# Kernel optimization log

Hardware: AMD Instinct MI355X
Metric: run time of the kernel (lower is better)

Reference implementation:

```python
import jax, jax.numpy as jnp
import numpy as np

N, E = 50000, 800000
IN_DIM, OUT_DIM, REL_DIM = 128, 64, 32
NEG_SLOPE = 0.01  # torch F.leaky_relu default


def setup_inputs() -> dict:
    key = jax.random.key(0)
    ks = jax.random.split(key, 12)
    return {
        "h": jax.random.normal(ks[0], (N, IN_DIM), jnp.float32),
        "relation": jax.random.normal(ks[1], (E, REL_DIM), jnp.float32),
        "score": jax.random.normal(ks[2], (E, 1), jnp.float32),
        "timestamp": jax.random.normal(ks[3], (E, 1), jnp.float32),
        "src": jax.random.randint(ks[4], (E,), 0, N, jnp.int32),
        "dst": jax.random.randint(ks[5], (E,), 0, N, jnp.int32),
        "W_n": jax.random.normal(ks[6], (IN_DIM, OUT_DIM), jnp.float32) / np.sqrt(IN_DIM),
        "W_r": jax.random.normal(ks[7], (REL_DIM, OUT_DIM), jnp.float32) / np.sqrt(REL_DIM),
        "W_s": jax.random.normal(ks[8], (1, OUT_DIM), jnp.float32),
        "W_t": jax.random.normal(ks[9], (1, OUT_DIM), jnp.float32),
        "a": jax.random.normal(ks[10], (5 * OUT_DIM,), jnp.float32) / np.sqrt(5 * OUT_DIM),
    }


def reference(h, relation, score, timestamp, src, dst, W_n, W_r, W_s, W_t, a):
    D = W_n.shape[1]
    z = h @ W_n                     # (N, D)
    er = relation @ W_r             # (E, D)
    es = score @ W_s                # (E, D)
    et = timestamp @ W_t            # (E, D)
    z_src = z[src]                  # (E, D) gather
    z_dst = z[dst]                  # (E, D) gather
    # attn_fc on concat([z_src, z_dst, er, es, et]) == sum of slice dot-products
    a1, a2, a3, a4, a5 = (a[0:D], a[D:2*D], a[2*D:3*D], a[3*D:4*D], a[4*D:5*D])
    logit = z_src @ a1 + z_dst @ a2 + er @ a3 + es @ a4 + et @ a5  # (E,)
    logit = jnp.where(logit >= 0, logit, NEG_SLOPE * logit)        # leaky_relu
    # segment softmax over edges grouped by dst node
    n = z.shape[0]
    seg_max = jax.ops.segment_max(logit, dst, num_segments=n)     # (N,)
    ex = jnp.exp(logit - seg_max[dst])                             # (E,)
    seg_sum = jax.ops.segment_sum(ex, dst, num_segments=n)        # (N,)
    alpha = ex / seg_sum[dst]                                      # (E,)
    # weighted scatter-sum of source features to dst nodes
    h_out = jax.ops.segment_sum(alpha[:, None] * z_src, dst, num_segments=n)  # (N, D)
    return h_out
```

## Files before the change

kernel.cpp:

```cpp
#include <hip/hip_runtime.h>

#define IN_DIM 128
#define OUT_DIM 64
#define REL_DIM 32
#define NEG_SLOPE 0.01f
#define CAP 64

__global__ void k_consts(const float* __restrict__ W_r, const float* __restrict__ W_s,
                         const float* __restrict__ W_t, const float* __restrict__ a,
                         float* __restrict__ consts ) {
    int t = threadIdx.x;
    if (t < REL_DIM) {
        const float* a3 = a + 2 * OUT_DIM;
        float acc = 0.f;
        for (int d = 0; d < OUT_DIM; ++d) acc += W_r[t * OUT_DIM + d] * a3[d];
        consts[t] = acc;
    } else if (t == 32) {
        float acc = 0.f;
        for (int d = 0; d < OUT_DIM; ++d) acc += W_s[d] * a[3 * OUT_DIM + d];
        consts[32] = acc;
    } else if (t == 33) {
        float acc = 0.f;
        for (int d = 0; d < OUT_DIM; ++d) acc += W_t[d] * a[4 * OUT_DIM + d];
        consts[33] = acc;
    }
}

__global__ __launch_bounds__(256) void k_node(const float* __restrict__ h,
                                              const float* __restrict__ W_n,
                                              const float* __restrict__ a,
                                              float* __restrict__ z,
                                              float* __restrict__ s1,
                                              float* __restrict__ s2, int n) {
    __shared__ float hs[IN_DIM * 65];
    __shared__ float s1p[4][64], s2p[4][64];
    int base = blockIdx.x * 64;

    for (int i = threadIdx.x; i < 64 * 32; i += 256) {
        int r = i >> 5;
        int c4 = i & 31;
        float4 v = make_float4(0.f, 0.f, 0.f, 0.f);
        if (base + r < n) v = ((const float4*)(h + (size_t)(base + r) * IN_DIM))[c4];
        int k0 = c4 * 4;
        hs[(k0 + 0) * 65 + r] = v.x;
        hs[(k0 + 1) * 65 + r] = v.y;
        hs[(k0 + 2) * 65 + r] = v.z;
        hs[(k0 + 3) * 65 + r] = v.w;
    }
    __syncthreads();

    int lane = threadIdx.x & 63;
    int w = __builtin_amdgcn_readfirstlane(threadIdx.x >> 6);
    int c0 = w * 16;
    int row = base + lane;

    float acc[16];
    #pragma unroll
    for (int j = 0; j < 16; ++j) acc[j] = 0.f;

    const float* __restrict__ Wslice = W_n + c0;
    #pragma unroll 4
    for (int k = 0; k < IN_DIM; ++k) {
        float hv = hs[k * 65 + lane];
        const float* __restrict__ Wr = Wslice + k * OUT_DIM;
        #pragma unroll
        for (int j = 0; j < 16; ++j) acc[j] = fmaf(hv, Wr[j], acc[j]);
    }

    float p1 = 0.f, p2 = 0.f;
    #pragma unroll
    for (int j = 0; j < 16; ++j) {
        p1 = fmaf(acc[j], a[c0 + j], p1);
        p2 = fmaf(acc[j], a[OUT_DIM + c0 + j], p2);
    }
    s1p[w][lane] = p1;
    s2p[w][lane] = p2;

    if (row < n) {
        float4* zp = (float4*)(z + (size_t)row * OUT_DIM + c0);
        zp[0] = make_float4(acc[0], acc[1], acc[2], acc[3]);
        zp[1] = make_float4(acc[4], acc[5], acc[6], acc[7]);
        zp[2] = make_float4(acc[8], acc[9], acc[10], acc[11]);
        zp[3] = make_float4(acc[12], acc[13], acc[14], acc[15]);
    }
    __syncthreads();
    if (threadIdx.x < 64 && base + (int)threadIdx.x < n) {
        int l = threadIdx.x;
        s1[base + l] = s1p[0][l] + s1p[1][l] + s1p[2][l] + s1p[3][l];
        s2[base + l] = s2p[0][l] + s2p[1][l] + s2p[2][l] + s2p[3][l];
    }
}

__global__ __launch_bounds__(256) void k_fill(const float* __restrict__ rel,
                                              const float* __restrict__ score,
                                              const float* __restrict__ ts,
                                              const int* __restrict__ src,
                                              const int* __restrict__ dst,
                                              const float* __restrict__ s1,
                                              const float* __restrict__ s2,
                                              const float* __restrict__ consts,
                                              int* __restrict__ cnt,
                                              int2* __restrict__ pedge, int E) {
    int tid = blockIdx.x * 256 + threadIdx.x;
    int e = tid >> 3;
    int sub = tid & 7;
    if (e >= E) return;

    float4 w = ((const float4*)consts)[sub];
    float4 v = ((const float4*)rel)[(size_t)e * 8 + sub];
    float dot = v.x * w.x + v.y * w.y + v.z * w.z + v.w * w.w;
    dot += __shfl_xor(dot, 1, 8);
    dot += __shfl_xor(dot, 2, 8);
    dot += __shfl_xor(dot, 4, 8);

    if (sub == 0) {
        int s = src[e], d = dst[e];
        float lg = dot + s1[s] + s2[d] + score[e] * consts[32] + ts[e] * consts[33];
        lg = (lg >= 0.f) ? lg : NEG_SLOPE * lg;
        int rank = atomicAdd(cnt + d, 1);
        if (rank < CAP)
            pedge[((size_t)d << 6) + rank] = make_int2(s, __float_as_int(lg));
    }
}

__global__ __launch_bounds__(256) void k_out(const int* __restrict__ cnt,
                                             const int2* __restrict__ pedge,
                                             const float* __restrict__ z,
                                             float* __restrict__ out, int n) {
    int lane = threadIdx.x & 63;
    int wave = (blockIdx.x * blockDim.x + threadIdx.x) >> 6;
    int nwaves = (gridDim.x * blockDim.x) >> 6;
    int eg = lane >> 4;
    int dl = lane & 15;
    for (int node = wave; node < n; node += nwaves) {
        int deg = min(cnt[node], CAP);
        float4 acc = make_float4(0.f, 0.f, 0.f, 0.f);
        if (deg > 0) {
            int2 pe = make_int2(0, (int)0xff800000u);
            if (lane < deg) pe = pedge[((size_t)node << 6) + lane];
            float v = __int_as_float(pe.y);
            float m = v;
            #pragma unroll
            for (int o = 32; o > 0; o >>= 1) m = fmaxf(m, __shfl_xor(m, o, 64));
            float ex = __expf(v - m);
            float ssum = ex;
            #pragma unroll
            for (int o = 32; o > 0; o >>= 1) ssum += __shfl_xor(ssum, o, 64);
            float alpha = ex * (1.0f / ssum);
            for (int j0 = 0; j0 < deg; j0 += 4) {
                int j = j0 + eg;
                int jc = (j < 64) ? j : 63;
                float wj = __shfl(alpha, jc, 64);
                int  sj = __shfl(pe.x, jc, 64);
                if (j < deg) {
                    float4 zv = ((const float4*)(z + (size_t)sj * OUT_DIM))[dl];
                    acc.x = fmaf(wj, zv.x, acc.x);
                    acc.y = fmaf(wj, zv.y, acc.y);
                    acc.z = fmaf(wj, zv.z, acc.z);
                    acc.w = fmaf(wj, zv.w, acc.w);
                }
            }
        }
        #pragma unroll
        for (int o = 16; o <= 32; o <<= 1) {
            acc.x += __shfl_xor(acc.x, o, 64);
            acc.y += __shfl_xor(acc.y, o, 64);
            acc.z += __shfl_xor(acc.z, o, 64);
            acc.w += __shfl_xor(acc.w, o, 64);
        }
        if (eg == 0) ((float4*)(out + (size_t)node * OUT_DIM))[dl] = acc;
    }
}

extern "C" void kernel_launch(void* const* d_in, const int* in_sizes, int n_in,
                              void* d_out, int out_size, void* d_ws, size_t ws_size,
                              hipStream_t stream) {
    const float* h         = (const float*)d_in[0];
    const float* relation  = (const float*)d_in[1];
    const float* score     = (const float*)d_in[2];
    const float* timestamp = (const float*)d_in[3];
    const int*   src       = (const int*)d_in[4];
    const int*   dst       = (const int*)d_in[5];
    const float* W_n       = (const float*)d_in[6];
    const float* W_r       = (const float*)d_in[7];
    const float* W_s       = (const float*)d_in[8];
    const float* W_t       = (const float*)d_in[9];
    const float* a         = (const float*)d_in[10];

    int n = in_sizes[0] / IN_DIM;
    int E = in_sizes[4];

    float* ws      = (float*)d_ws;
    float* z       = ws;
    float* s1      = z + (size_t)n * OUT_DIM;
    float* s2      = s1 + n;
    float* consts  = s2 + n;
    int*   cnt     = (int*)(consts + 64);
    int2*  pedge   = (int2*)(cnt + n);

    float* out = (float*)d_out;

    hipMemsetAsync(cnt, 0, (size_t)n * sizeof(int), stream);

    k_consts<<<1, 64, 0, stream>>>(W_r, W_s, W_t, a, consts);
    k_node<<<(n + 63) / 64, 256, 0, stream>>>(h, W_n, a, z, s1, s2, n);
    int nfb = (int)(((long long)E * 8 + 255) / 256);
    k_fill<<<nfb, 256, 0, stream>>>(relation, score, timestamp, src, dst,
                                    s1, s2, consts, cnt, pedge, E);
    k_out<<<(n + 3) / 4, 256, 0, stream>>>(cnt, pedge, z, out, n);
}
```

Before: 282.0 us.

## Split edge fill into logit pass and dst-range-partitioned bucketing pass

Edge processing is split into two kernels. The first computes each edge's logit and writes a packed (dst<<16|src, logit) record into the output buffer, used here as scratch. The second has 8 groups of blocks each scan all records but handle only one range of dst nodes, so atomics and pedge writes touch a smaller working set that fits better in cache. In exchange, every block group rereads the whole record array and there is an extra kernel launch. The 16-bit packing of src and dst also breaks for N above 65536; with N=50000 it fits.

Result: slower. 297.9 us (+5.7%).

```diff
diff --git a/kernel.cpp b/kernel.cpp
--- a/kernel.cpp
+++ b/kernel.cpp
@@ -5,6 +5,7 @@
 #define REL_DIM 32
 #define NEG_SLOPE 0.01f
 #define CAP 64
+#define NB 8
 
 __global__ void k_consts(const float* __restrict__ W_r, const float* __restrict__ W_s,
                          const float* __restrict__ W_t, const float* __restrict__ a,
@@ -91,16 +92,15 @@
     }
 }
 
-__global__ __launch_bounds__(256) void k_fill(const float* __restrict__ rel,
-                                              const float* __restrict__ score,
-                                              const float* __restrict__ ts,
-                                              const int* __restrict__ src,
-                                              const int* __restrict__ dst,
-                                              const float* __restrict__ s1,
-                                              const float* __restrict__ s2,
-                                              const float* __restrict__ consts,
-                                              int* __restrict__ cnt,
-                                              int2* __restrict__ pedge, int E) {
+__global__ __launch_bounds__(256) void k_edgeA(const float* __restrict__ rel,
+                                               const float* __restrict__ score,
+                                               const float* __restrict__ ts,
+                                               const int* __restrict__ src,
+                                               const int* __restrict__ dst,
+                                               const float* __restrict__ s1,
+                                               const float* __restrict__ s2,
+                                               const float* __restrict__ consts,
+                                               int2* __restrict__ rec, int E) {
     int tid = blockIdx.x * 256 + threadIdx.x;
     int e = tid >> 3;
     int sub = tid & 7;
@@ -117,9 +117,31 @@
         int s = src[e], d = dst[e];
         float lg = dot + s1[s] + s2[d] + score[e] * consts[32] + ts[e] * consts[33];
         lg = (lg >= 0.f) ? lg : NEG_SLOPE * lg;
-        int rank = atomicAdd(cnt + d, 1);
-        if (rank < CAP)
-            pedge[((size_t)d << 6) + rank] = make_int2(s, __float_as_int(lg));
+        unsigned key = ((unsigned)d << 16) | (unsigned)s;
+        rec[e] = make_int2((int)key, __float_as_int(lg));
+    }
+}
+
+__global__ __launch_bounds__(256) void k_edgeB(const int2* __restrict__ rec,
+                                               int* __restrict__ cnt,
+                                               int2* __restrict__ pedge,
+                                               int E, int n, int npg) {
+    int g = blockIdx.x & (NB - 1);
+    int chunk = blockIdx.x >> 3;
+    int nchunk = gridDim.x >> 3;
+    int lo = g * npg;
+    int hi = min(n, lo + npg);
+    int per = (E + nchunk - 1) / nchunk;
+    int cs = chunk * per;
+    int ce = min(E, cs + per);
+    for (int i = cs + threadIdx.x; i < ce; i += 256) {
+        int2 r = rec[i];
+        int d = (int)(((unsigned)r.x) >> 16);
+        if (d >= lo && d < hi) {
+            int rank = atomicAdd(cnt + d, 1);
+            if (rank < CAP)
+                pedge[((size_t)d << 6) + rank] = make_int2(r.x & 0xffff, r.y);
+        }
     }
 }
 
@@ -198,14 +220,20 @@
     int*   cnt     = (int*)(consts + 64);
     int2*  pedge   = (int2*)(cnt + n);
 
+    int2* rec = (int2*)d_out;
     float* out = (float*)d_out;
 
     hipMemsetAsync(cnt, 0, (size_t)n * sizeof(int), stream);
 
     k_consts<<<1, 64, 0, stream>>>(W_r, W_s, W_t, a, consts);
     k_node<<<(n + 63) / 64, 256, 0, stream>>>(h, W_n, a, z, s1, s2, n);
-    int nfb = (int)(((long long)E * 8 + 255) / 256);
-    k_fill<<<nfb, 256, 0, stream>>>(relation, score, timestamp, src, dst,
-                                    s1, s2, consts, cnt, pedge, E);
+
+    int nab = (int)(((long long)E * 8 + 255) / 256);
+    k_edgeA<<<nab, 256, 0, stream>>>(relation, score, timestamp, src, dst,
+                                     s1, s2, consts, rec, E);
+
+    int npg = (n + NB - 1) / NB;
+    k_edgeB<<<2048, 256, 0, stream>>>(rec, cnt, pedge, E, n, npg);
+
     k_out<<<(n + 3) / 4, 256, 0, stream>>>(cnt, pedge, z, out, n);
 }
```

## Bucket edges by destination block with block-local histograms and shared-memory segment sort

Applied to the files above, without the earlier changes.

Replaces per-node global atomics and fixed 64-slot per-node edge slots with a two-level bucketing. Each fill block builds a shared-memory histogram over 64-node buckets, reserves space with one global atomic per bucket, and writes packed (dst,src,logit) records. The output kernel then loads one bucket per block and sorts its records into per-node shared-memory lists before doing the softmax and gather. The consts kernel and the memset are folded into other kernels, which cuts launches and scattered global atomics. In exchange it packs src and dst into 16 bits each, which breaks once n exceeds 65536, caps buckets at 1536 edges, and leans on zeroing bcnt in k_node block 0 while other k_node blocks run.

Result: slower. 297.8 us (+5.6%).

```diff
diff --git a/kernel.cpp b/kernel.cpp
--- a/kernel.cpp
+++ b/kernel.cpp
@@ -5,36 +5,23 @@
 #define REL_DIM 32
 #define NEG_SLOPE 0.01f
 #define CAP 64
-
-__global__ void k_consts(const float* __restrict__ W_r, const float* __restrict__ W_s,
-                         const float* __restrict__ W_t, const float* __restrict__ a,
-                         float* __restrict__ consts ) {
-    int t = threadIdx.x;
-    if (t < REL_DIM) {
-        const float* a3 = a + 2 * OUT_DIM;
-        float acc = 0.f;
-        for (int d = 0; d < OUT_DIM; ++d) acc += W_r[t * OUT_DIM + d] * a3[d];
-        consts[t] = acc;
-    } else if (t == 32) {
-        float acc = 0.f;
-        for (int d = 0; d < OUT_DIM; ++d) acc += W_s[d] * a[3 * OUT_DIM + d];
-        consts[32] = acc;
-    } else if (t == 33) {
-        float acc = 0.f;
-        for (int d = 0; d < OUT_DIM; ++d) acc += W_t[d] * a[4 * OUT_DIM + d];
-        consts[33] = acc;
-    }
-}
+#define FB_EDGES 2048
+#define BCAP 1536
+#define MAXB 1024
 
 __global__ __launch_bounds__(256) void k_node(const float* __restrict__ h,
                                               const float* __restrict__ W_n,
                                               const float* __restrict__ a,
                                               float* __restrict__ z,
                                               float* __restrict__ s1,
-                                              float* __restrict__ s2, int n) {
+                                              float* __restrict__ s2,
+                                              int* __restrict__ bcnt, int n) {
     __shared__ float hs[IN_DIM * 65];
     __shared__ float s1p[4][64], s2p[4][64];
     int base = blockIdx.x * 64;
+
+    if (blockIdx.x == 0)
+        for (int i = threadIdx.x; i < MAXB; i += 256) bcnt[i] = 0;
 
     for (int i = threadIdx.x; i < 64 * 32; i += 256) {
         int r = i >> 5;
@@ -91,53 +78,128 @@
     }
 }
 
-__global__ __launch_bounds__(256) void k_fill(const float* __restrict__ rel,
-                                              const float* __restrict__ score,
-                                              const float* __restrict__ ts,
-                                              const int* __restrict__ src,
-                                              const int* __restrict__ dst,
-                                              const float* __restrict__ s1,
-                                              const float* __restrict__ s2,
-                                              const float* __restrict__ consts,
-                                              int* __restrict__ cnt,
-                                              int2* __restrict__ pedge, int E) {
-    int tid = blockIdx.x * 256 + threadIdx.x;
-    int e = tid >> 3;
+__global__ __launch_bounds__(512) void k_fillP(const float* __restrict__ rel,
+                                               const float* __restrict__ score,
+                                               const float* __restrict__ ts,
+                                               const int* __restrict__ src,
+                                               const int* __restrict__ dst,
+                                               const float* __restrict__ s1,
+                                               const float* __restrict__ s2,
+                                               const float* __restrict__ W_r,
+                                               const float* __restrict__ W_s,
+                                               const float* __restrict__ W_t,
+                                               const float* __restrict__ a,
+                                               int* __restrict__ bcnt,
+                                               int2* __restrict__ rec2,
+                                               int E, int nbkt) {
+    __shared__ float cw[REL_DIM + 2];
+    __shared__ int2  stage[FB_EDGES];
+    __shared__ int   sinfo[FB_EDGES];
+    __shared__ int   lhist[MAXB];
+    __shared__ int   lbase[MAXB];
+    int tid = threadIdx.x;
+
+    if (tid < REL_DIM) {
+        const float* a3 = a + 2 * OUT_DIM;
+        float acc = 0.f;
+        #pragma unroll
+        for (int d2 = 0; d2 < OUT_DIM; ++d2)
+            acc = fmaf(W_r[tid * OUT_DIM + d2], a3[d2], acc);
+        cw[tid] = acc;
+    } else if (tid == 32) {
+        float acc = 0.f;
+        for (int d2 = 0; d2 < OUT_DIM; ++d2) acc = fmaf(W_s[d2], a[3 * OUT_DIM + d2], acc);
+        cw[32] = acc;
+    } else if (tid == 33) {
+        float acc = 0.f;
+        for (int d2 = 0; d2 < OUT_DIM; ++d2) acc = fmaf(W_t[d2], a[4 * OUT_DIM + d2], acc);
+        cw[33] = acc;
+    }
+    for (int i = tid; i < nbkt; i += 512) lhist[i] = 0;
+    __syncthreads();
+
+    int e0 = blockIdx.x * FB_EDGES;
+    int g = tid >> 3;
     int sub = tid & 7;
-    if (e >= E) return;
-
-    float4 w = ((const float4*)consts)[sub];
-    float4 v = ((const float4*)rel)[(size_t)e * 8 + sub];
-    float dot = v.x * w.x + v.y * w.y + v.z * w.z + v.w * w.w;
-    dot += __shfl_xor(dot, 1, 8);
-    dot += __shfl_xor(dot, 2, 8);
-    dot += __shfl_xor(dot, 4, 8);
-
-    if (sub == 0) {
-        int s = src[e], d = dst[e];
-        float lg = dot + s1[s] + s2[d] + score[e] * consts[32] + ts[e] * consts[33];
-        lg = (lg >= 0.f) ? lg : NEG_SLOPE * lg;
-        int rank = atomicAdd(cnt + d, 1);
-        if (rank < CAP)
-            pedge[((size_t)d << 6) + rank] = make_int2(s, __float_as_int(lg));
-    }
-}
-
-__global__ __launch_bounds__(256) void k_out(const int* __restrict__ cnt,
-                                             const int2* __restrict__ pedge,
-                                             const float* __restrict__ z,
-                                             float* __restrict__ out, int n) {
-    int lane = threadIdx.x & 63;
-    int wave = (blockIdx.x * blockDim.x + threadIdx.x) >> 6;
-    int nwaves = (gridDim.x * blockDim.x) >> 6;
+
+    #pragma unroll 1
+    for (int it = 0; it < FB_EDGES / 64; ++it) {
+        int le = it * 64 + g;
+        int e = e0 + le;
+        if (e < E) {
+            float4 w4 = ((const float4*)cw)[sub];
+            float4 v = ((const float4*)rel)[(size_t)e * 8 + sub];
+            float dot = v.x * w4.x + v.y * w4.y + v.z * w4.z + v.w * w4.w;
+            dot += __shfl_xor(dot, 1, 8);
+            dot += __shfl_xor(dot, 2, 8);
+            dot += __shfl_xor(dot, 4, 8);
+            if (sub == 0) {
+                int s = src[e], d = dst[e];
+                float lg = dot + s1[s] + s2[d] + score[e] * cw[32] + ts[e] * cw[33];
+                lg = (lg >= 0.f) ? lg : NEG_SLOPE * lg;
+                int b = d >> 6;
+                int lr = atomicAdd(&lhist[b], 1);
+                stage[le] = make_int2((int)(((unsigned)d << 16) | (unsigned)s),
+                                      __float_as_int(lg));
+                sinfo[le] = (lr << 12) | b;
+            }
+        }
+    }
+    __syncthreads();
+
+    for (int b = tid; b < nbkt; b += 512) {
+        int c = lhist[b];
+        if (c > 0) lbase[b] = atomicAdd(bcnt + b, c);
+    }
+    __syncthreads();
+
+    for (int le = tid; le < FB_EDGES; le += 512) {
+        int e = e0 + le;
+        if (e < E) {
+            int info = sinfo[le];
+            int b = info & 0xFFF;
+            int lr = info >> 12;
+            int pos = lbase[b] + lr;
+            if (pos < BCAP) rec2[(size_t)b * BCAP + pos] = stage[le];
+        }
+    }
+}
+
+__global__ __launch_bounds__(256) void k_out2(const int* __restrict__ bcnt,
+                                              const int2* __restrict__ rec2,
+                                              const float* __restrict__ z,
+                                              float* __restrict__ out, int n) {
+    __shared__ int2 seg[64][CAP];
+    __shared__ int scnt[64];
+    int b = blockIdx.x;
+    int tid = threadIdx.x;
+    if (tid < 64) scnt[tid] = 0;
+    __syncthreads();
+
+    int cnt = bcnt[b];
+    if (cnt > BCAP) cnt = BCAP;
+    const int2* rb = rec2 + (size_t)b * BCAP;
+    for (int i = tid; i < cnt; i += 256) {
+        int2 r = rb[i];
+        int dl = (int)((((unsigned)r.x) >> 16) & 63u);
+        int rk = atomicAdd(&scnt[dl], 1);
+        if (rk < CAP) seg[dl][rk] = make_int2(r.x & 0xffff, r.y);
+    }
+    __syncthreads();
+
+    int lane = tid & 63;
+    int w = tid >> 6;
     int eg = lane >> 4;
-    int dl = lane & 15;
-    for (int node = wave; node < n; node += nwaves) {
-        int deg = min(cnt[node], CAP);
+    int dl4 = lane & 15;
+    for (int k = 0; k < 16; ++k) {
+        int dl = w * 16 + k;
+        int node = b * 64 + dl;
+        if (node >= n) break;
+        int deg = min(scnt[dl], CAP);
         float4 acc = make_float4(0.f, 0.f, 0.f, 0.f);
         if (deg > 0) {
             int2 pe = make_int2(0, (int)0xff800000u);
-            if (lane < deg) pe = pedge[((size_t)node << 6) + lane];
+            if (lane < deg) pe = seg[dl][lane];
             float v = __int_as_float(pe.y);
             float m = v;
             #pragma unroll
@@ -151,9 +213,9 @@
                 int j = j0 + eg;
                 int jc = (j < 64) ? j : 63;
                 float wj = __shfl(alpha, jc, 64);
-                int  sj = __shfl(pe.x, jc, 64);
+                int sj = __shfl(pe.x, jc, 64);
                 if (j < deg) {
-                    float4 zv = ((const float4*)(z + (size_t)sj * OUT_DIM))[dl];
+                    float4 zv = ((const float4*)(z + (size_t)sj * OUT_DIM))[dl4];
                     acc.x = fmaf(wj, zv.x, acc.x);
                     acc.y = fmaf(wj, zv.y, acc.y);
                     acc.z = fmaf(wj, zv.z, acc.z);
@@ -168,7 +230,7 @@
             acc.z += __shfl_xor(acc.z, o, 64);
             acc.w += __shfl_xor(acc.w, o, 64);
         }
-        if (eg == 0) ((float4*)(out + (size_t)node * OUT_DIM))[dl] = acc;
+        if (eg == 0) ((float4*)(out + (size_t)node * OUT_DIM))[dl4] = acc;
     }
 }
 
@@ -189,23 +251,22 @@
 
     int n = in_sizes[0] / IN_DIM;
     int E = in_sizes[4];
-
-    float* ws      = (float*)d_ws;
-    float* z       = ws;
-    float* s1      = z + (size_t)n * OUT_DIM;
-    float* s2      = s1 + n;
-    float* consts  = s2 + n;
-    int*   cnt     = (int*)(consts + 64);
-    int2*  pedge   = (int2*)(cnt + n);
+    int nbkt = (n + 63) >> 6;
+
+    float* ws   = (float*)d_ws;
+    float* z    = ws;
+    float* s1   = z + (size_t)n * OUT_DIM;
+    float* s2   = s1 + n;
+    int*   bcnt = (int*)(s2 + n);
+    int2*  rec2 = (int2*)(bcnt + MAXB);
 
     float* out = (float*)d_out;
 
-    hipMemsetAsync(cnt, 0, (size_t)n * sizeof(int), stream);
-
-    k_consts<<<1, 64, 0, stream>>>(W_r, W_s, W_t, a, consts);
-    k_node<<<(n + 63) / 64, 256, 0, stream>>>(h, W_n, a, z, s1, s2, n);
-    int nfb = (int)(((long long)E * 8 + 255) / 256);
-    k_fill<<<nfb, 256, 0, stream>>>(relation, score, timestamp, src, dst,
-                                    s1, s2, consts, cnt, pedge, E);
-    k_out<<<(n + 3) / 4, 256, 0, stream>>>(cnt, pedge, z, out, n);
-}
+    k_node<<<(n + 63) / 64, 256, 0, stream>>>(h, W_n, a, z, s1, s2, bcnt, n);
+
+    int nfb = (E + FB_EDGES - 1) / FB_EDGES;
+    k_fillP<<<nfb, 512, 0, stream>>>(relation, score, timestamp, src, dst,
+                                     s1, s2, W_r, W_s, W_t, a, bcnt, rec2, E, nbkt);
+
+    k_out2<<<nbkt, 256, 0, stream>>>(bcnt, rec2, z, out, n);
+}
```
